# Performance work log

Hardware: AMD Instinct MI355X
Metric: run time of the kernel (lower is better)

Reference implementation:

```python
import jax, jax.numpy as jnp
import numpy as np

SEQ_LEN = 262144
N = 128  # number of event types


def setup_inputs() -> dict:
    key = jax.random.key(0)
    k_in, k_q, k_k = jax.random.split(key, 3)
    scale = 1.0 / np.sqrt(N)  # matches nn.Linear default init scale
    Input = jax.random.normal(k_in, (SEQ_LEN, N), dtype=jnp.float32)
    W_Q = jax.random.uniform(k_q, (N, N), dtype=jnp.float32, minval=-scale, maxval=scale)
    W_K = jax.random.uniform(k_k, (N, N), dtype=jnp.float32, minval=-scale, maxval=scale)
    return {"Input": Input, "W_Q": W_Q, "W_K": W_K}


def reference(Input, W_Q, W_K):
    # Original loops over one-hot type rows e_t:
    #   query_t = e_t @ W_Q.T = W_Q[:, t]
    #   keys    = Input @ W_K.T                         (S, N)
    #   aw[:,t] = softplus(keys @ query_t)
    #   Output[s,t] = aw[s,t] * sum_j Input[s,j]
    # Fused/batched form:
    keys = Input @ W_K.T                                 # (S, N)
    aw = jax.nn.softplus(keys @ W_Q)                     # (S, N), col t uses W_Q[:, t]
    row_sum = jnp.sum(Input, axis=1, keepdims=True)      # (S, 1)
    Output = aw * row_sum                                # (S, N)
    loss = jnp.mean((Output[:-1] - Input[1:]) ** 2)
    l1 = jnp.sum(jnp.abs(jax.nn.sigmoid(W_K.T @ W_Q)))
    return (loss, l1)
```

## Files before the change

kernel.cpp:

```cpp
#include <hip/hip_runtime.h>
#include <math.h>

#define S_LEN 262144
#define N 128
#define BR 64
#define TPB 256

typedef __attribute__((ext_vector_type(8))) short bf16x8;
typedef __attribute__((ext_vector_type(4))) float f32x4;

__device__ __forceinline__ unsigned short f2bf(float x) {
    unsigned b = __float_as_uint(x);
    b = (b + 0x7FFF + ((b >> 16) & 1)) >> 16;
    return (unsigned short)b;
}

__device__ __forceinline__ float wave_reduce(float v) {
    #pragma unroll
    for (int off = 32; off > 0; off >>= 1) v += __shfl_down(v, off, 64);
    return v;
}

__global__ void mk_kernel(const float* __restrict__ WQ, const float* __restrict__ WK,
                          unsigned short* __restrict__ fragB, float* __restrict__ out) {
    const int i = blockIdx.x;
    const int j = threadIdx.x;
    float acc = 0.f;
    #pragma unroll 8
    for (int r = 0; r < N; ++r) acc = fmaf(WK[r * N + i], WQ[r * N + j], acc);

    const int kk = i >> 5, q = (i >> 3) & 3, jj = i & 7;
    const int ct = j >> 4, n15 = j & 15;
    fragB[((kk * 8 + ct) * 64 + (q * 16 + n15)) * 8 + jj] = f2bf(acc);

    float sg = fabsf(1.0f / (1.0f + __expf(-acc)));
    float ws = wave_reduce(sg);
    __shared__ float red[2];
    if ((j & 63) == 0) red[j >> 6] = ws;
    __syncthreads();
    if (j == 0) atomicAdd(&out[1], red[0] + red[1]);
}

__global__ __launch_bounds__(TPB, 4) void main_kernel(
    const float* __restrict__ In, const unsigned short* __restrict__ fragB,
    float* __restrict__ out, float inv_denom) {
    __shared__ unsigned short sA[BR][136];
    __shared__ float sPartF[BR][33];
    __shared__ float sPart[BR][4];
    __shared__ float sRed[TPB / 64];

    const int tid = threadIdx.x;
    const int w = tid >> 6, lane = tid & 63;
    const int q = lane >> 4, n15 = lane & 15;
    const long r0 = (long)blockIdx.x * BR;

    bf16x8 bF[2][4];
    #pragma unroll
    for (int c = 0; c < 2; ++c)
        #pragma unroll
        for (int kk = 0; kk < 4; ++kk)
            bF[c][kk] = *(const bf16x8*)&fragB[((kk * 8 + (w * 2 + c)) * 64 + lane) * 8];

    #pragma unroll
    for (int t = 0; t < 8; ++t) {
        const int qq = tid + t * TPB;
        const int r = qq >> 5;
        const int c4 = (qq & 31) << 2;
        const float4 v = *(const float4*)&In[(r0 + r) * N + c4];
        ushort4 h;
        h.x = f2bf(v.x); h.y = f2bf(v.y); h.z = f2bf(v.z); h.w = f2bf(v.w);
        *(ushort4*)&sA[r][c4] = h;
        sPartF[r][qq & 31] = v.x + v.y + v.z + v.w;
    }
    __syncthreads();

    {
        const int r = tid >> 2, sg = (tid & 3) << 3;
        float s = 0.f;
        #pragma unroll
        for (int e = 0; e < 8; ++e) s += sPartF[r][sg + e];
        sPart[r][tid & 3] = s;
    }

    f32x4 acc[4][2];
    #pragma unroll
    for (int rt = 0; rt < 4; ++rt)
        #pragma unroll
        for (int c = 0; c < 2; ++c) acc[rt][c] = (f32x4){0.f, 0.f, 0.f, 0.f};

    #pragma unroll
    for (int rt = 0; rt < 4; ++rt) {
        #pragma unroll
        for (int kk = 0; kk < 4; ++kk) {
            bf16x8 a = *(const bf16x8*)&sA[rt * 16 + n15][kk * 32 + q * 8];
            #pragma unroll
            for (int c = 0; c < 2; ++c)
                acc[rt][c] = __builtin_amdgcn_mfma_f32_16x16x32_bf16(a, bF[c][kk], acc[rt][c], 0, 0, 0);
        }
    }
    __syncthreads();

    float lsum = 0.f;
    #pragma unroll
    for (int rt = 0; rt < 4; ++rt) {
        #pragma unroll
        for (int reg = 0; reg < 4; ++reg) {
            const int row = rt * 16 + q * 4 + reg;
            const float4 p = *(const float4*)&sPart[row][0];
            const float rs = p.x + p.y + p.z + p.w;
            const long s = r0 + row;
            const bool has = (s < S_LEN - 1);
            #pragma unroll
            for (int c = 0; c < 2; ++c) {
                const float z = acc[rt][c][reg];
                const float sp = fmaxf(z, 0.f) + __logf(1.0f + __expf(-fabsf(z)));
                const float o = sp * rs;
                if (has) {
                    const int col = w * 32 + c * 16 + n15;
                    const float d = o - In[(s + 1) * N + col];
                    lsum = fmaf(d, d, lsum);
                }
            }
        }
    }

    const float wsum = wave_reduce(lsum);
    if ((tid & 63) == 0) sRed[w] = wsum;
    __syncthreads();
    if (tid == 0) {
        float t = 0.f;
        #pragma unroll
        for (int w2 = 0; w2 < TPB / 64; ++w2) t += sRed[w2];
        atomicAdd(&out[0], t * inv_denom);
    }
}

extern "C" void kernel_launch(void* const* d_in, const int* in_sizes, int n_in,
                              void* d_out, int out_size, void* d_ws, size_t ws_size,
                              hipStream_t stream) {
    const float* In = (const float*)d_in[0];
    const float* WQ = (const float*)d_in[1];
    const float* WK = (const float*)d_in[2];
    float* out = (float*)d_out;
    unsigned short* fragB = (unsigned short*)d_ws;

    hipMemsetAsync(d_out, 0, 2 * sizeof(float), stream);
    mk_kernel<<<128, 128, 0, stream>>>(WQ, WK, fragB, out);
    const float inv = (float)(1.0 / ((double)(S_LEN - 1) * (double)N));
    main_kernel<<<S_LEN / BR, TPB, 0, stream>>>(In, fragB, out, inv);
}
```

Before: 234.1 us.

## Persistent grid with register double-buffered tile prefetch and shared-memory loss targets

Switches to a persistent grid of 1024 blocks that loop over row tiles. The next tile's input is prefetched into registers while the current tile is converted, multiplied with MFMA and reduced. The loss target row is now read from the bf16 shared-memory copy (with one extra halo row) instead of a second global fp32 read. It also uses a cheaper bf16 packing via perm, which drops round-to-nearest-even. Targets are rounded to bf16, which slightly changes loss precision, and occupancy bounds drop to 3 blocks.

```diff
diff --git a/kernel.cpp b/kernel.cpp
--- a/kernel.cpp
+++ b/kernel.cpp
@@ -5,6 +5,8 @@
 #define N 128
 #define BR 64
 #define TPB 256
+#define NT (S_LEN / BR)
+#define GRID 1024
 
 typedef __attribute__((ext_vector_type(8))) short bf16x8;
 typedef __attribute__((ext_vector_type(4))) float f32x4;
@@ -14,7 +16,13 @@
     b = (b + 0x7FFF + ((b >> 16) & 1)) >> 16;
     return (unsigned short)b;
 }
-
+__device__ __forceinline__ float bf2f(unsigned short u) {
+    return __uint_as_float((unsigned)u << 16);
+}
+__device__ __forceinline__ unsigned pack2bf(float x, float y) {
+    return __builtin_amdgcn_perm(__float_as_uint(y) + 0x8000u,
+                                 __float_as_uint(x) + 0x8000u, 0x07060302u);
+}
 __device__ __forceinline__ float wave_reduce(float v) {
     #pragma unroll
     for (int off = 32; off > 0; off >>= 1) v += __shfl_down(v, off, 64);
@@ -41,18 +49,17 @@
     if (j == 0) atomicAdd(&out[1], red[0] + red[1]);
 }
 
-__global__ __launch_bounds__(TPB, 4) void main_kernel(
+__global__ __launch_bounds__(TPB, 3) void main_kernel(
     const float* __restrict__ In, const unsigned short* __restrict__ fragB,
     float* __restrict__ out, float inv_denom) {
-    __shared__ unsigned short sA[BR][136];
-    __shared__ float sPartF[BR][33];
-    __shared__ float sPart[BR][4];
+    __shared__ unsigned short sA[65][136];
+    __shared__ float sPartF[64][33];
+    __shared__ float sPart[64][4];
     __shared__ float sRed[TPB / 64];
 
     const int tid = threadIdx.x;
     const int w = tid >> 6, lane = tid & 63;
     const int q = lane >> 4, n15 = lane & 15;
-    const long r0 = (long)blockIdx.x * BR;
 
     bf16x8 bF[2][4];
     #pragma unroll
@@ -61,67 +68,99 @@
         for (int kk = 0; kk < 4; ++kk)
             bF[c][kk] = *(const bf16x8*)&fragB[((kk * 8 + (w * 2 + c)) * 64 + lane) * 8];
 
-    #pragma unroll
-    for (int t = 0; t < 8; ++t) {
-        const int qq = tid + t * TPB;
-        const int r = qq >> 5;
-        const int c4 = (qq & 31) << 2;
-        const float4 v = *(const float4*)&In[(r0 + r) * N + c4];
-        ushort4 h;
-        h.x = f2bf(v.x); h.y = f2bf(v.y); h.z = f2bf(v.z); h.w = f2bf(v.w);
-        *(ushort4*)&sA[r][c4] = h;
-        sPartF[r][qq & 31] = v.x + v.y + v.z + v.w;
-    }
-    __syncthreads();
+    float4 buf0[8], buf1[8], x0, x1;
+    float lsum = 0.f;
 
-    {
-        const int r = tid >> 2, sg = (tid & 3) << 3;
-        float s = 0.f;
+    auto issue = [&](float4 (&b)[8], float4& x, int tile) {
+        const long r0 = (long)tile * BR;
         #pragma unroll
-        for (int e = 0; e < 8; ++e) s += sPartF[r][sg + e];
-        sPart[r][tid & 3] = s;
-    }
+        for (int t = 0; t < 8; ++t) {
+            const int qq = tid + t * TPB;
+            const int r = qq >> 5, c4 = (qq & 31) << 2;
+            b[t] = *(const float4*)&In[(r0 + r) * N + c4];
+        }
+        if (tid < 32) {
+            long rX = r0 + 64; if (rX > S_LEN - 1) rX = S_LEN - 1;
+            x = *(const float4*)&In[rX * N + (tid << 2)];
+        }
+    };
 
-    f32x4 acc[4][2];
-    #pragma unroll
-    for (int rt = 0; rt < 4; ++rt)
+    auto compute = [&](float4 (&b)[8], float4& x, int tile) {
+        const long r0 = (long)tile * BR;
         #pragma unroll
-        for (int c = 0; c < 2; ++c) acc[rt][c] = (f32x4){0.f, 0.f, 0.f, 0.f};
+        for (int t = 0; t < 8; ++t) {
+            const int qq = tid + t * TPB;
+            const int r = qq >> 5, c4 = (qq & 31) << 2;
+            uint2 pk = make_uint2(pack2bf(b[t].x, b[t].y), pack2bf(b[t].z, b[t].w));
+            *(uint2*)&sA[r][c4] = pk;
+            sPartF[r][qq & 31] = b[t].x + b[t].y + b[t].z + b[t].w;
+        }
+        if (tid < 32)
+            *(uint2*)&sA[64][tid << 2] = make_uint2(pack2bf(x.x, x.y), pack2bf(x.z, x.w));
+        __syncthreads();
 
-    #pragma unroll
-    for (int rt = 0; rt < 4; ++rt) {
+        {
+            const int r = tid >> 2, sg0 = (tid & 3) << 3;
+            float s = 0.f;
+            #pragma unroll
+            for (int e = 0; e < 8; ++e) s += sPartF[r][sg0 + e];
+            sPart[r][tid & 3] = s;
+        }
+
+        f32x4 acc[4][2];
         #pragma unroll
-        for (int kk = 0; kk < 4; ++kk) {
-            bf16x8 a = *(const bf16x8*)&sA[rt * 16 + n15][kk * 32 + q * 8];
+        for (int rt = 0; rt < 4; ++rt)
             #pragma unroll
-            for (int c = 0; c < 2; ++c)
-                acc[rt][c] = __builtin_amdgcn_mfma_f32_16x16x32_bf16(a, bF[c][kk], acc[rt][c], 0, 0, 0);
+            for (int c = 0; c < 2; ++c) acc[rt][c] = (f32x4){0.f, 0.f, 0.f, 0.f};
+        #pragma unroll
+        for (int rt = 0; rt < 4; ++rt) {
+            #pragma unroll
+            for (int kk = 0; kk < 4; ++kk) {
+                bf16x8 a = *(const bf16x8*)&sA[rt * 16 + n15][kk * 32 + q * 8];
+                #pragma unroll
+                for (int c = 0; c < 2; ++c)
+                    acc[rt][c] = __builtin_amdgcn_mfma_f32_16x16x32_bf16(a, bF[c][kk], acc[rt][c], 0, 0, 0);
+            }
         }
-    }
-    __syncthreads();
+        __syncthreads();
 
-    float lsum = 0.f;
-    #pragma unroll
-    for (int rt = 0; rt < 4; ++rt) {
         #pragma unroll
-        for (int reg = 0; reg < 4; ++reg) {
-            const int row = rt * 16 + q * 4 + reg;
-            const float4 p = *(const float4*)&sPart[row][0];
-            const float rs = p.x + p.y + p.z + p.w;
-            const long s = r0 + row;
-            const bool has = (s < S_LEN - 1);
+        for (int rt = 0; rt < 4; ++rt) {
             #pragma unroll
-            for (int c = 0; c < 2; ++c) {
-                const float z = acc[rt][c][reg];
-                const float sp = fmaxf(z, 0.f) + __logf(1.0f + __expf(-fabsf(z)));
-                const float o = sp * rs;
-                if (has) {
-                    const int col = w * 32 + c * 16 + n15;
-                    const float d = o - In[(s + 1) * N + col];
-                    lsum = fmaf(d, d, lsum);
+            for (int reg = 0; reg < 4; ++reg) {
+                const int row = rt * 16 + q * 4 + reg;
+                const float4 p = *(const float4*)&sPart[row][0];
+                const float rs = p.x + p.y + p.z + p.w;
+                const long s = r0 + row;
+                const bool has = (s < S_LEN - 1);
+                #pragma unroll
+                for (int c = 0; c < 2; ++c) {
+                    const float z = acc[rt][c][reg];
+                    const float sp = fmaxf(z, 0.f) + __logf(1.0f + __expf(-fabsf(z)));
+                    const float o = sp * rs;
+                    if (has) {
+                        const int col = w * 32 + c * 16 + n15;
+                        const float d = o - bf2f(sA[row + 1][col]);
+                        lsum = fmaf(d, d, lsum);
+                    }
                 }
             }
         }
+        __syncthreads();
+    };
+
+    int t0 = blockIdx.x;
+    issue(buf0, x0, t0);
+    while (t0 < NT) {
+        const int t1 = t0 + GRID;
+        if (t1 < NT) issue(buf1, x1, t1);
+        compute(buf0, x0, t0);
+        t0 = t1;
+        if (t0 >= NT) break;
+        const int t2 = t0 + GRID;
+        if (t2 < NT) issue(buf0, x0, t2);
+        compute(buf1, x1, t0);
+        t0 = t2;
     }
 
     const float wsum = wave_reduce(lsum);
@@ -147,5 +186,5 @@
     hipMemsetAsync(d_out, 0, 2 * sizeof(float), stream);
     mk_kernel<<<128, 128, 0, stream>>>(WQ, WK, fragB, out);
     const float inv = (float)(1.0 / ((double)(S_LEN - 1) * (double)N));
-    main_kernel<<<S_LEN / BR, TPB, 0, stream>>>(In, fragB, out, inv);
+    main_kernel<<<GRID, TPB, 0, stream>>>(In, fragB, out, inv);
 }
```

Measured after the change: 283.5 us. +21.1%, slower.

## Use persistent per-wave tiles with register prefetch and MFMA row sums

Applied to the files above, without the earlier changes.

The main kernel becomes a persistent grid. Each wave loops over 16-row by 64-column items and prefetches the next item's input into registers while it computes the current one. Row sums now come from an MFMA against a bf16 ones vector, and the next-row loss target is read from the bf16 copy in LDS instead of being re-read from global memory. Block-wide barriers are replaced with per-wave LDS waits. In exchange, each 16-row tile is loaded by two waves, and both the targets and the row sums pick up bf16 rounding error.

```diff
diff --git a/kernel.cpp b/kernel.cpp
--- a/kernel.cpp
+++ b/kernel.cpp
@@ -3,8 +3,10 @@
 
 #define S_LEN 262144
 #define N 128
-#define BR 64
 #define TPB 256
+#define GRID 768
+#define NWAVES (GRID * 4)
+#define ITEMS (S_LEN / 16 * 2)
 
 typedef __attribute__((ext_vector_type(8))) short bf16x8;
 typedef __attribute__((ext_vector_type(4))) float f32x4;
@@ -14,11 +16,20 @@
     b = (b + 0x7FFF + ((b >> 16) & 1)) >> 16;
     return (unsigned short)b;
 }
-
+__device__ __forceinline__ float bf2f(unsigned short u) {
+    return __uint_as_float((unsigned)u << 16);
+}
+__device__ __forceinline__ unsigned pack2bf(float x, float y) {
+    return __builtin_amdgcn_perm(__float_as_uint(y) + 0x8000u,
+                                 __float_as_uint(x) + 0x8000u, 0x07060302u);
+}
 __device__ __forceinline__ float wave_reduce(float v) {
     #pragma unroll
     for (int off = 32; off > 0; off >>= 1) v += __shfl_down(v, off, 64);
     return v;
+}
+__device__ __forceinline__ void lds_fence() {
+    asm volatile("s_waitcnt lgkmcnt(0)" ::: "memory");
 }
 
 __global__ void mk_kernel(const float* __restrict__ WQ, const float* __restrict__ WK,
@@ -41,87 +52,98 @@
     if (j == 0) atomicAdd(&out[1], red[0] + red[1]);
 }
 
-__global__ __launch_bounds__(TPB, 4) void main_kernel(
+__global__ __launch_bounds__(TPB, 3) void main_kernel(
     const float* __restrict__ In, const unsigned short* __restrict__ fragB,
     float* __restrict__ out, float inv_denom) {
-    __shared__ unsigned short sA[BR][136];
-    __shared__ float sPartF[BR][33];
-    __shared__ float sPart[BR][4];
-    __shared__ float sRed[TPB / 64];
+    __shared__ unsigned short sA[4][17][132];
+    __shared__ float sRed[4];
 
     const int tid = threadIdx.x;
     const int w = tid >> 6, lane = tid & 63;
     const int q = lane >> 4, n15 = lane & 15;
-    const long r0 = (long)blockIdx.x * BR;
+    const int gid = blockIdx.x * 4 + w;
+    const int half = gid & 1;
 
-    bf16x8 bF[2][4];
+    bf16x8 bF[4][4];
     #pragma unroll
-    for (int c = 0; c < 2; ++c)
+    for (int c4 = 0; c4 < 4; ++c4)
         #pragma unroll
         for (int kk = 0; kk < 4; ++kk)
-            bF[c][kk] = *(const bf16x8*)&fragB[((kk * 8 + (w * 2 + c)) * 64 + lane) * 8];
+            bF[c4][kk] = *(const bf16x8*)&fragB[((kk * 8 + (half * 4 + c4)) * 64 + lane) * 8];
 
+    bf16x8 bOne;
     #pragma unroll
-    for (int t = 0; t < 8; ++t) {
-        const int qq = tid + t * TPB;
-        const int r = qq >> 5;
-        const int c4 = (qq & 31) << 2;
-        const float4 v = *(const float4*)&In[(r0 + r) * N + c4];
-        ushort4 h;
-        h.x = f2bf(v.x); h.y = f2bf(v.y); h.z = f2bf(v.z); h.w = f2bf(v.w);
-        *(ushort4*)&sA[r][c4] = h;
-        sPartF[r][qq & 31] = v.x + v.y + v.z + v.w;
-    }
-    __syncthreads();
+    for (int e = 0; e < 8; ++e) bOne[e] = (short)0x3F80;
 
-    {
-        const int r = tid >> 2, sg = (tid & 3) << 3;
-        float s = 0.f;
+    unsigned short (*my)[132] = sA[w];
+    float lsum = 0.f;
+    float4 r[8];
+    float2 x;
+
+    auto issue = [&](int item) {
+        const long r0 = (long)(item >> 1) * 16;
+        const float* base = In + r0 * N;
         #pragma unroll
-        for (int e = 0; e < 8; ++e) s += sPartF[r][sg + e];
-        sPart[r][tid & 3] = s;
-    }
+        for (int j = 0; j < 8; ++j)
+            r[j] = *(const float4*)(base + j * 256 + lane * 4);
+        long rX = r0 + 16; if (rX > S_LEN - 1) rX = S_LEN - 1;
+        x = *(const float2*)&In[rX * N + lane * 2];
+    };
 
-    f32x4 acc[4][2];
-    #pragma unroll
-    for (int rt = 0; rt < 4; ++rt)
+    int item = gid;
+    issue(item);
+
+    while (item < ITEMS) {
+        const int next = item + NWAVES;
+
         #pragma unroll
-        for (int c = 0; c < 2; ++c) acc[rt][c] = (f32x4){0.f, 0.f, 0.f, 0.f};
+        for (int j = 0; j < 8; ++j) {
+            const int row = 2 * j + (lane >> 5);
+            const int c = lane & 31;
+            *(unsigned int*)&my[row][c * 4] = pack2bf(r[j].x, r[j].y);
+            *(unsigned int*)&my[row][c * 4 + 2] = pack2bf(r[j].z, r[j].w);
+        }
+        *(unsigned int*)&my[16][lane * 2] = pack2bf(x.x, x.y);
 
-    #pragma unroll
-    for (int rt = 0; rt < 4; ++rt) {
+        if (next < ITEMS) issue(next);
+
+        lds_fence();
+
+        f32x4 acc[4], aRS;
+        aRS = (f32x4){0.f, 0.f, 0.f, 0.f};
+        #pragma unroll
+        for (int c4 = 0; c4 < 4; ++c4) acc[c4] = (f32x4){0.f, 0.f, 0.f, 0.f};
         #pragma unroll
         for (int kk = 0; kk < 4; ++kk) {
-            bf16x8 a = *(const bf16x8*)&sA[rt * 16 + n15][kk * 32 + q * 8];
+            bf16x8 a = *(const bf16x8*)&my[n15][kk * 32 + q * 8];
+            aRS = __builtin_amdgcn_mfma_f32_16x16x32_bf16(a, bOne, aRS, 0, 0, 0);
             #pragma unroll
-            for (int c = 0; c < 2; ++c)
-                acc[rt][c] = __builtin_amdgcn_mfma_f32_16x16x32_bf16(a, bF[c][kk], acc[rt][c], 0, 0, 0);
+            for (int c4 = 0; c4 < 4; ++c4)
+                acc[c4] = __builtin_amdgcn_mfma_f32_16x16x32_bf16(a, bF[c4][kk], acc[c4], 0, 0, 0);
         }
-    }
-    __syncthreads();
 
-    float lsum = 0.f;
-    #pragma unroll
-    for (int rt = 0; rt < 4; ++rt) {
+        const long r0 = (long)(item >> 1) * 16;
         #pragma unroll
         for (int reg = 0; reg < 4; ++reg) {
-            const int row = rt * 16 + q * 4 + reg;
-            const float4 p = *(const float4*)&sPart[row][0];
-            const float rs = p.x + p.y + p.z + p.w;
+            const int row = q * 4 + reg;
+            const float rs = aRS[reg];
             const long s = r0 + row;
             const bool has = (s < S_LEN - 1);
             #pragma unroll
-            for (int c = 0; c < 2; ++c) {
-                const float z = acc[rt][c][reg];
+            for (int c4 = 0; c4 < 4; ++c4) {
+                const float z = acc[c4][reg];
                 const float sp = fmaxf(z, 0.f) + __logf(1.0f + __expf(-fabsf(z)));
                 const float o = sp * rs;
                 if (has) {
-                    const int col = w * 32 + c * 16 + n15;
-                    const float d = o - In[(s + 1) * N + col];
+                    const int col = half * 64 + c4 * 16 + n15;
+                    const float d = o - bf2f(my[row + 1][col]);
                     lsum = fmaf(d, d, lsum);
                 }
             }
         }
+
+        lds_fence();
+        item = next;
     }
 
     const float wsum = wave_reduce(lsum);
@@ -130,7 +152,7 @@
     if (tid == 0) {
         float t = 0.f;
         #pragma unroll
-        for (int w2 = 0; w2 < TPB / 64; ++w2) t += sRed[w2];
+        for (int w2 = 0; w2 < 4; ++w2) t += sRed[w2];
         atomicAdd(&out[0], t * inv_denom);
     }
 }
@@ -147,5 +169,5 @@
     hipMemsetAsync(d_out, 0, 2 * sizeof(float), stream);
     mk_kernel<<<128, 128, 0, stream>>>(WQ, WK, fragB, out);
     const float inv = (float)(1.0 / ((double)(S_LEN - 1) * (double)N));
-    main_kernel<<<S_LEN / BR, TPB, 0, stream>>>(In, fragB, out, inv);
+    main_kernel<<<GRID, TPB, 0, stream>>>(In, fragB, out, inv);
 }
```

Result: faster. 205.2 us (-12.4%).
